# Performance work log

Measured on AMD Instinct MI355X. Metric: run time of the kernel, lower is better.

Reference implementation:

```python
import jax, jax.numpy as jnp
import numpy as np

B, S, E, H, ML = 4, 1024, 1024, 16, 2048
HD = E // H


def setup_inputs() -> dict:
    key = jax.random.key(0)
    ks = jax.random.split(key, 8)
    s = 0.02
    return {
        "x": jax.random.normal(ks[0], (B, S, E), dtype=jnp.float32),
        "rel_pos": jax.random.normal(ks[1], (H, ML), dtype=jnp.float32),
        "in_proj_w": jax.random.normal(ks[2], (3 * E, E), dtype=jnp.float32) * s,
        "in_proj_b": jnp.zeros((3 * E,), jnp.float32),
        "out_w": jax.random.normal(ks[3], (E, E), dtype=jnp.float32) * s,
        "out_b": jnp.zeros((E,), jnp.float32),
        "w1": jax.random.normal(ks[4], (4 * E, E), dtype=jnp.float32) * s,
        "b1": jnp.zeros((4 * E,), jnp.float32),
        "w2": jax.random.normal(ks[5], (E, 4 * E), dtype=jnp.float32) * s,
        "b2": jnp.zeros((E,), jnp.float32),
        "ln1_g": jnp.ones((E,), jnp.float32),
        "ln1_b": jnp.zeros((E,), jnp.float32),
        "ln2_g": jnp.ones((E,), jnp.float32),
        "ln2_b": jnp.zeros((E,), jnp.float32),
    }


def _layernorm(x, g, b, eps=1e-5):
    m = x.mean(-1, keepdims=True)
    v = ((x - m) ** 2).mean(-1, keepdims=True)
    return (x - m) * jax.lax.rsqrt(v + eps) * g + b


def _causal_mask(size, rel_pos):
    # rel_pos: [H, max_len]; size <= max_len branch of the torch code
    flipped = jnp.flip(rel_pos[:, :size], -1)                        # [H, size]
    neg_inf = jnp.full((rel_pos.shape[0], size), -jnp.inf, rel_pos.dtype)
    padded = jnp.concatenate([flipped, neg_inf], axis=-1)            # [H, 2*size]
    idx = jnp.arange(size)[None, :] - jnp.arange(size)[:, None] + size - 1
    return padded[:, idx]                                            # [H, S, S]: rel_pos[i-j] if j<=i else -inf


def reference(x, rel_pos, in_proj_w, in_proj_b, out_w, out_b,
              w1, b1, w2, b2, ln1_g, ln1_b, ln2_g, ln2_b):
    b, s, e = x.shape
    xn = _layernorm(x, ln1_g, ln1_b)
    qkv = xn @ in_proj_w.T + in_proj_b                               # [B,S,3E]
    q, k, v = jnp.split(qkv, 3, axis=-1)
    q = q.reshape(b, s, H, HD).transpose(0, 2, 1, 3)                 # [B,H,S,D]
    k = k.reshape(b, s, H, HD).transpose(0, 2, 1, 3)
    v = v.reshape(b, s, H, HD).transpose(0, 2, 1, 3)
    mask = _causal_mask(s, rel_pos)                                  # [H,S,S], broadcast over batch (== repeat(B,1,1))
    scores = jnp.einsum("bhqd,bhkd->bhqk", q, k) / np.sqrt(HD) + mask[None]
    attn = jax.nn.softmax(scores, axis=-1)
    o = jnp.einsum("bhqk,bhkd->bhqd", attn, v)                       # [B,H,S,D]
    o = o.transpose(0, 2, 1, 3).reshape(b, s, e)
    att_out = o @ out_w.T + out_b
    x = x + att_out
    xm = _layernorm(x, ln2_g, ln2_b)
    mlp = jax.nn.relu(xm @ w1.T + b1) @ w2.T + b2
    return x + mlp
```

## Files before the change

### kernel.cpp

```cpp
#include <hip/hip_runtime.h>
#include <stdint.h>

typedef __bf16 bf16x8 __attribute__((ext_vector_type(8)));
typedef float  f32x4  __attribute__((ext_vector_type(4)));

__device__ __forceinline__ unsigned short f2bf(float f) {
  union { float f; unsigned int u; } a; a.f = f;
  unsigned int r = a.u + 0x7FFFu + ((a.u >> 16) & 1u);
  return (unsigned short)(r >> 16);
}

__device__ __forceinline__ unsigned short f2bf_fast(float f) {
  union { __bf16 b; unsigned short u; } v; v.b = (__bf16)f; return v.u;
}

__device__ __forceinline__ void cp16(const void* g, void* l) {
  auto g1 = reinterpret_cast<__attribute__((address_space(1))) unsigned int*>(
      reinterpret_cast<uintptr_t>(g));
  auto l3 = reinterpret_cast<__attribute__((address_space(3))) unsigned int*>(
      reinterpret_cast<uintptr_t>(l));
  __builtin_amdgcn_global_load_lds(g1, l3, 16, 0, 0);
}

__global__ __launch_bounds__(256) void cvt_bf16(const float* __restrict__ in,
                                                unsigned short* __restrict__ out,
                                                int n) {
  int i = (blockIdx.x * 256 + threadIdx.x) * 4;
  if (i >= n) return;
  float4 v = *(const float4*)(in + i);
  union { unsigned short u[4]; uint2 p; } o;
  o.u[0] = f2bf(v.x); o.u[1] = f2bf(v.y); o.u[2] = f2bf(v.z); o.u[3] = f2bf(v.w);
  *(uint2*)(out + i) = o.p;
}

__global__ __launch_bounds__(256) void init_br(const float* __restrict__ resid,
                                               const float* __restrict__ bias,
                                               float* __restrict__ out) {
  int i = (blockIdx.x * 256 + threadIdx.x) * 4;
  float4 r = *(const float4*)(resid + i);
  float4 b = *(const float4*)(bias + (i & 1023));
  r.x += b.x; r.y += b.y; r.z += b.z; r.w += b.w;
  *(float4*)(out + i) = r;
}

__global__ __launch_bounds__(256) void ln_bf16(const float* __restrict__ x,
                                               const float* __restrict__ g,
                                               const float* __restrict__ bta,
                                               unsigned short* __restrict__ out) {
  const int row = blockIdx.x, t = threadIdx.x;
  const float4 v = *(const float4*)(x + (size_t)row * 1024 + t * 4);
  float s1 = v.x + v.y + v.z + v.w;
  float s2 = v.x*v.x + v.y*v.y + v.z*v.z + v.w*v.w;
  #pragma unroll
  for (int off = 1; off < 64; off <<= 1) {
    s1 += __shfl_xor(s1, off, 64);
    s2 += __shfl_xor(s2, off, 64);
  }
  __shared__ float r1[4], r2[4];
  if ((t & 63) == 0) { r1[t >> 6] = s1; r2[t >> 6] = s2; }
  __syncthreads();
  s1 = r1[0] + r1[1] + r1[2] + r1[3];
  s2 = r2[0] + r2[1] + r2[2] + r2[3];
  const float mean = s1 * (1.0f / 1024.0f);
  const float var  = s2 * (1.0f / 1024.0f) - mean * mean;
  const float rstd = rsqrtf(var + 1e-5f);
  const float4 gv = *(const float4*)(g + t * 4);
  const float4 bv = *(const float4*)(bta + t * 4);
  union { unsigned short u[4]; uint2 p; } o;
  o.u[0] = f2bf((v.x - mean) * rstd * gv.x + bv.x);
  o.u[1] = f2bf((v.y - mean) * rstd * gv.y + bv.y);
  o.u[2] = f2bf((v.z - mean) * rstd * gv.z + bv.z);
  o.u[3] = f2bf((v.w - mean) * rstd * gv.w + bv.w);
  *(uint2*)(out + (size_t)row * 1024 + t * 4) = o.p;
}

template <int MODE>
__global__ __launch_bounds__(256, 2) void gemm_bt(
    const unsigned short* __restrict__ A,
    const unsigned short* __restrict__ Bt,
    const float* __restrict__ bias,
    void* __restrict__ outp,
    int N, int K) {
  __shared__ __align__(16) unsigned short As[128 * 64];
  __shared__ __align__(16) unsigned short Bs[128 * 64];
  const int tid = threadIdx.x;
  const int wave = tid >> 6, lane = tid & 63;
  const int q = lane >> 4, c = lane & 15;
  const int wm = (wave & 1) << 6, wn = (wave >> 1) << 6;
  const int m0 = blockIdx.x << 7, n0 = blockIdx.y << 7;

  const int srow = tid >> 3;
  const int cg8  = ((tid & 7) ^ (srow & 7)) << 3;

  const unsigned short* gA = A  + (size_t)(m0 + srow) * K + cg8;
  const unsigned short* gB = Bt + (size_t)(n0 + srow) * K + cg8;
  unsigned short* lA = &As[tid * 8];
  unsigned short* lB = &Bs[tid * 8];
  const size_t rstep = (size_t)32 * K;

  const f32x4 fzero = {0.f, 0.f, 0.f, 0.f};
  f32x4 acc[4][4];
  #pragma unroll
  for (int i = 0; i < 4; i++)
    #pragma unroll
    for (int j = 0; j < 4; j++) acc[i][j] = fzero;

  for (int k0 = 0; k0 < K; k0 += 64) {
    __syncthreads();
    #pragma unroll
    for (int it = 0; it < 4; it++) {
      cp16(gA + it * rstep + k0, lA + it * 2048);
      cp16(gB + it * rstep + k0, lB + it * 2048);
    }
    __syncthreads();
    #pragma unroll
    for (int ks = 0; ks < 2; ks++) {
      const int sw = (((ks << 2) + q) ^ (c & 7)) << 3;
      bf16x8 af[4], bf[4];
      #pragma unroll
      for (int i = 0; i < 4; i++) af[i] = *(const bf16x8*)&As[(wm + i*16 + c)*64 + sw];
      #pragma unroll
      for (int j = 0; j < 4; j++) bf[j] = *(const bf16x8*)&Bs[(wn + j*16 + c)*64 + sw];
      #pragma unroll
      for (int i = 0; i < 4; i++)
        #pragma unroll
        for (int j = 0; j < 4; j++)
          acc[i][j] = __builtin_amdgcn_mfma_f32_16x16x32_bf16(af[i], bf[j], acc[i][j], 0, 0, 0);
    }
  }

  float bj[4];
  #pragma unroll
  for (int j = 0; j < 4; j++) bj[j] = bias[n0 + wn + j * 16 + c];
  #pragma unroll
  for (int i = 0; i < 4; i++) {
    #pragma unroll
    for (int r = 0; r < 4; r++) {
      const int row = m0 + wm + i * 16 + q * 4 + r;
      #pragma unroll
      for (int j = 0; j < 4; j++) {
        const int col = n0 + wn + j * 16 + c;
        const size_t idx = (size_t)row * N + col;
        float v = acc[i][j][r] + bj[j];
        if (MODE == 0)      ((unsigned short*)outp)[idx] = f2bf(v);
        else                ((unsigned short*)outp)[idx] = f2bf(fmaxf(v, 0.f));
      }
    }
  }
}

__global__ __launch_bounds__(256, 2) void gemm_bt_splitk(
    const unsigned short* __restrict__ A,
    const unsigned short* __restrict__ Bt,
    float* __restrict__ outp,
    int N, int K) {
  __shared__ __align__(16) unsigned short As[128 * 64];
  __shared__ __align__(16) unsigned short Bs[128 * 64];
  const int tid = threadIdx.x;
  const int wave = tid >> 6, lane = tid & 63;
  const int q = lane >> 4, c = lane & 15;
  const int wm = (wave & 1) << 6, wn = (wave >> 1) << 6;
  const int m0 = blockIdx.x << 7, n0 = blockIdx.y << 7;
  const int KH = K >> 1;
  const int kbeg = blockIdx.z * KH, kend = kbeg + KH;

  const int srow = tid >> 3;
  const int cg8  = ((tid & 7) ^ (srow & 7)) << 3;

  const unsigned short* gA = A  + (size_t)(m0 + srow) * K + cg8;
  const unsigned short* gB = Bt + (size_t)(n0 + srow) * K + cg8;
  unsigned short* lA = &As[tid * 8];
  unsigned short* lB = &Bs[tid * 8];
  const size_t rstep = (size_t)32 * K;

  const f32x4 fzero = {0.f, 0.f, 0.f, 0.f};
  f32x4 acc[4][4];
  #pragma unroll
  for (int i = 0; i < 4; i++)
    #pragma unroll
    for (int j = 0; j < 4; j++) acc[i][j] = fzero;

  for (int k0 = kbeg; k0 < kend; k0 += 64) {
    __syncthreads();
    #pragma unroll
    for (int it = 0; it < 4; it++) {
      cp16(gA + it * rstep + k0, lA + it * 2048);
      cp16(gB + it * rstep + k0, lB + it * 2048);
    }
    __syncthreads();
    #pragma unroll
    for (int ks = 0; ks < 2; ks++) {
      const int sw = (((ks << 2) + q) ^ (c & 7)) << 3;
      bf16x8 af[4], bf[4];
      #pragma unroll
      for (int i = 0; i < 4; i++) af[i] = *(const bf16x8*)&As[(wm + i*16 + c)*64 + sw];
      #pragma unroll
      for (int j = 0; j < 4; j++) bf[j] = *(const bf16x8*)&Bs[(wn + j*16 + c)*64 + sw];
      #pragma unroll
      for (int i = 0; i < 4; i++)
        #pragma unroll
        for (int j = 0; j < 4; j++)
          acc[i][j] = __builtin_amdgcn_mfma_f32_16x16x32_bf16(af[i], bf[j], acc[i][j], 0, 0, 0);
    }
  }

  #pragma unroll
  for (int i = 0; i < 4; i++) {
    #pragma unroll
    for (int r = 0; r < 4; r++) {
      const int row = m0 + wm + i * 16 + q * 4 + r;
      #pragma unroll
      for (int j = 0; j < 4; j++) {
        const int col = n0 + wn + j * 16 + c;
        atomicAdd(outp + (size_t)row * N + col, acc[i][j][r]);
      }
    }
  }
}

__global__ __launch_bounds__(256, 2) void attn_flash(
    const unsigned short* __restrict__ qkv,
    const float* __restrict__ rel_pos,
    unsigned short* __restrict__ o) {
  __shared__ __align__(16) unsigned short Qs[128 * 64];
  __shared__ __align__(16) unsigned short Ks[64 * 64];
  __shared__ __align__(16) unsigned short Vs[64 * 64];
  __shared__ __align__(16) unsigned short Ps[4][32 * 64];
  __shared__ float rps[1024];

  const int tid = threadIdx.x;
  const int wave = tid >> 6, lane = tid & 63;
  const int q = lane >> 4, c = lane & 15;

  const int lid = blockIdx.x + (blockIdx.y << 3);
  const int xq = lid & 7, y = lid >> 3;
  const int qt = (y & 32) ? (7 - xq) : xq;
  const int b = y >> 4, h = y & 15;

  const unsigned short* qg = qkv + (size_t)b * 1024 * 3072 + h * 64;
  const unsigned short* kg = qg + 1024;
  const unsigned short* vg = qg + 2048;

  #pragma unroll
  for (int i = 0; i < 4; i++) {
    const int idx = tid + i * 256;
    rps[idx & 1023] = rel_pos[h * 2048 + (idx & 1023)] * 1.44269504f;
  }

  const int sr  = tid >> 3;
  const int cg8 = ((tid & 7) ^ (sr & 7)) << 3;
  #pragma unroll
  for (int it = 0; it < 4; it++)
    cp16(qg + (size_t)(qt * 128 + sr + it * 32) * 3072 + cg8, &Qs[(tid + it * 256) * 8]);
  __syncthreads();

  bf16x8 qf[2][2];
  #pragma unroll
  for (int mt = 0; mt < 2; mt++)
    #pragma unroll
    for (int ks = 0; ks < 2; ks++)
      qf[mt][ks] = *(const bf16x8*)&Qs[(wave*32 + mt*16 + c)*64 + ((((ks<<2)+q) ^ (c & 7)) << 3)];

  const f32x4 fzero = {0.f, 0.f, 0.f, 0.f};
  f32x4 O[2][4];
  float l_i[2][4];
  #pragma unroll
  for (int mt = 0; mt < 2; mt++) {
    #pragma unroll
    for (int r = 0; r < 4; r++) l_i[mt][r] = 0.f;
    #pragma unroll
    for (int dt = 0; dt < 4; dt++) O[mt][dt] = fzero;
  }

  unsigned short* Pw = &Ps[wave][0];
  const int i_base = qt * 128 + wave * 32;
  const int vrow = tid & 63, d0 = (tid >> 6) << 4;
  const int vchunk = vrow >> 3, vlo = vrow & 7;

  const float sc = 0.125f * 1.44269504f;
  const int kdiag = qt << 1;
  const int nkt = (qt + 1) * 2;

  for (int kt = 0; kt < nkt; kt++) {
    __syncthreads();
    cp16(kg + (size_t)(kt * 64 + sr) * 3072 + cg8, &Ks[tid * 8]);
    cp16(kg + (size_t)(kt * 64 + sr + 32) * 3072 + cg8, &Ks[(tid + 256) * 8]);
    {
      union { int4 v; unsigned short u[8]; } va, vb2;
      const unsigned short* vrp = vg + (size_t)(kt * 64 + vrow) * 3072 + d0;
      va.v  = *(const int4*)vrp;
      vb2.v = *(const int4*)(vrp + 8);
      #pragma unroll
      for (int j = 0; j < 8; j++) {
        const int pos = ((vchunk ^ j) << 3) + vlo;
        Vs[(d0 + j) * 64 + pos]     = va.u[j];
        Vs[(d0 + 8 + j) * 64 + pos] = vb2.u[j];
      }
    }
    __syncthreads();

    f32x4 S[2][4];
    #pragma unroll
    for (int mt = 0; mt < 2; mt++)
      #pragma unroll
      for (int nt = 0; nt < 4; nt++) S[mt][nt] = fzero;
    #pragma unroll
    for (int ks = 0; ks < 2; ks++) {
      const int sw = (((ks << 2) + q) ^ (c & 7)) << 3;
      bf16x8 kb[4];
      #pragma unroll
      for (int nt = 0; nt < 4; nt++) kb[nt] = *(const bf16x8*)&Ks[(nt*16 + c)*64 + sw];
      #pragma unroll
      for (int mt = 0; mt < 2; mt++)
        #pragma unroll
        for (int nt = 0; nt < 4; nt++)
          S[mt][nt] = __builtin_amdgcn_mfma_f32_16x16x32_bf16(qf[mt][ks], kb[nt], S[mt][nt], 0, 0, 0);
    }

    if (kt < kdiag) {
      #pragma unroll
      for (int mt = 0; mt < 2; mt++) {
        #pragma unroll
        for (int r = 0; r < 4; r++) {
          const int i_ = i_base + mt * 16 + q * 4 + r;
          const int prow = (mt * 16 + q * 4 + r) * 64;
          const int rsw  = (q * 4 + r) & 7;
          float s = 0.f;
          #pragma unroll
          for (int nt = 0; nt < 4; nt++) {
            const int j_ = kt * 64 + nt * 16 + c;
            const float p = exp2f(fmaf(S[mt][nt][r], sc, rps[i_ - j_]));
            s += p;
            Pw[prow + ((((nt << 1) + (c >> 3)) ^ rsw) << 3) + (c & 7)] = f2bf_fast(p);
          }
          l_i[mt][r] += s;
        }
      }
    } else {
      #pragma unroll
      for (int mt = 0; mt < 2; mt++) {
        #pragma unroll
        for (int r = 0; r < 4; r++) {
          const int i_ = i_base + mt * 16 + q * 4 + r;
          const int prow = (mt * 16 + q * 4 + r) * 64;
          const int rsw  = (q * 4 + r) & 7;
          float s = 0.f;
          #pragma unroll
          for (int nt = 0; nt < 4; nt++) {
            const int j_ = kt * 64 + nt * 16 + c;
            const int d_ = i_ - j_;
            const float p = (d_ >= 0)
                ? exp2f(fmaf(S[mt][nt][r], sc, rps[d_ & 1023])) : 0.f;
            s += p;
            Pw[prow + ((((nt << 1) + (c >> 3)) ^ rsw) << 3) + (c & 7)] = f2bf_fast(p);
          }
          l_i[mt][r] += s;
        }
      }
    }

    asm volatile("s_waitcnt lgkmcnt(0)" ::: "memory");

    #pragma unroll
    for (int ks = 0; ks < 2; ks++) {
      const int sw = (((ks << 2) + q) ^ (c & 7)) << 3;
      bf16x8 pa[2], vb[4];
      #pragma unroll
      for (int mt = 0; mt < 2; mt++) pa[mt] = *(const bf16x8*)&Pw[(mt*16 + c)*64 + sw];
      #pragma unroll
      for (int dt = 0; dt < 4; dt++) vb[dt] = *(const bf16x8*)&Vs[(dt*16 + c)*64 + sw];
      #pragma unroll
      for (int mt = 0; mt < 2; mt++)
        #pragma unroll
        for (int dt = 0; dt < 4; dt++)
          O[mt][dt] = __builtin_amdgcn_mfma_f32_16x16x32_bf16(pa[mt], vb[dt], O[mt][dt], 0, 0, 0);
    }
  }

  #pragma unroll
  for (int mt = 0; mt < 2; mt++) {
    #pragma unroll
    for (int r = 0; r < 4; r++) {
      float l = l_i[mt][r];
      l += __shfl_xor(l, 1, 64);
      l += __shfl_xor(l, 2, 64);
      l += __shfl_xor(l, 4, 64);
      l += __shfl_xor(l, 8, 64);
      const float inv = 1.0f / l;
      const int i_ = i_base + mt * 16 + q * 4 + r;
      unsigned short* orow = o + (size_t)(b * 1024 + i_) * 1024 + h * 64 + c;
      #pragma unroll
      for (int dt = 0; dt < 4; dt++) orow[dt * 16] = f2bf(O[mt][dt][r] * inv);
    }
  }
}

extern "C" void kernel_launch(void* const* d_in, const int* in_sizes, int n_in,
                              void* d_out, int out_size, void* d_ws, size_t ws_size,
                              hipStream_t stream) {
  (void)in_sizes; (void)n_in; (void)out_size; (void)ws_size;
  const float* x    = (const float*)d_in[0];
  const float* rel  = (const float*)d_in[1];
  const float* ipw  = (const float*)d_in[2];
  const float* ipb  = (const float*)d_in[3];
  const float* outw = (const float*)d_in[4];
  const float* outb = (const float*)d_in[5];
  const float* w1   = (const float*)d_in[6];
  const float* b1   = (const float*)d_in[7];
  const float* w2   = (const float*)d_in[8];
  const float* b2   = (const float*)d_in[9];
  const float* ln1g = (const float*)d_in[10];
  const float* ln1b = (const float*)d_in[11];
  const float* ln2g = (const float*)d_in[12];
  const float* ln2b = (const float*)d_in[13];

  unsigned short* ipw_b  = (unsigned short*)d_ws;
  unsigned short* outw_b = ipw_b  + (size_t)3072 * 1024;
  unsigned short* w1_b   = outw_b + (size_t)1024 * 1024;
  unsigned short* w2_b   = w1_b   + (size_t)4096 * 1024;
  unsigned short* xn     = w2_b   + (size_t)1024 * 4096;
  unsigned short* qkvb   = xn     + (size_t)4096 * 1024;
  unsigned short* ob     = qkvb   + (size_t)4096 * 3072;
  float*          x2     = (float*)(ob + (size_t)4096 * 1024);
  unsigned short* xm     = (unsigned short*)(x2 + (size_t)4096 * 1024);
  unsigned short* hb     = xm + (size_t)4096 * 1024;

  cvt_bf16<<<3072 * 1024 / 1024, 256, 0, stream>>>(ipw, ipw_b, 3072 * 1024);
  cvt_bf16<<<1024 * 1024 / 1024, 256, 0, stream>>>(outw, outw_b, 1024 * 1024);
  cvt_bf16<<<4096 * 1024 / 1024, 256, 0, stream>>>(w1, w1_b, 4096 * 1024);
  cvt_bf16<<<4096 * 1024 / 1024, 256, 0, stream>>>(w2, w2_b, 4096 * 1024);

  ln_bf16<<<4096, 256, 0, stream>>>(x, ln1g, ln1b, xn);

  gemm_bt<0><<<dim3(32, 24), 256, 0, stream>>>(xn, ipw_b, ipb, qkvb, 3072, 1024);

  attn_flash<<<dim3(8, 64), 256, 0, stream>>>(qkvb, rel, ob);

  init_br<<<4096, 256, 0, stream>>>(x, outb, x2);
  gemm_bt_splitk<<<dim3(32, 8, 2), 256, 0, stream>>>(ob, outw_b, x2, 1024, 1024);

  ln_bf16<<<4096, 256, 0, stream>>>(x2, ln2g, ln2b, xm);

  gemm_bt<2><<<dim3(32, 32), 256, 0, stream>>>(xm, w1_b, b1, hb, 4096, 1024);

  init_br<<<4096, 256, 0, stream>>>(x2, b2, (float*)d_out);
  gemm_bt_splitk<<<dim3(32, 8, 2), 256, 0, stream>>>(hb, w2_b, (float*)d_out, 1024, 4096);
}
```

Baseline: 347.9 us.

## Merge weight conversions, fold residual seeding into layernorm, deepen split-K

Replaces the four weight-conversion launches with one kernel that selects source and destination by index range. Folds the residual-plus-bias seeding into the layernorm kernels, which removes two init_br launches and one re-read of the activations each. Raises split-K from 2 to 4 ways for both output GEMMs and asks for higher occupancy in launch bounds. This launches more atomic-accumulating blocks, so atomic contention rises and floating-point summation order changes.

```diff
diff --git a/kernel.cpp b/kernel.cpp
--- a/kernel.cpp
+++ b/kernel.cpp
@@ -22,33 +22,39 @@
   __builtin_amdgcn_global_load_lds(g1, l3, 16, 0, 0);
 }
 
-__global__ __launch_bounds__(256) void cvt_bf16(const float* __restrict__ in,
-                                                unsigned short* __restrict__ out,
-                                                int n) {
+__global__ __launch_bounds__(256) void cvt_all(
+    const float* __restrict__ s0, const float* __restrict__ s1,
+    const float* __restrict__ s2, const float* __restrict__ s3,
+    unsigned short* __restrict__ d0, unsigned short* __restrict__ d1,
+    unsigned short* __restrict__ d2, unsigned short* __restrict__ d3) {
   int i = (blockIdx.x * 256 + threadIdx.x) * 4;
-  if (i >= n) return;
-  float4 v = *(const float4*)(in + i);
+  const float* src; unsigned short* dst; int off;
+  if (i < 3145728)       { src = s0; dst = d0; off = 0; }
+  else if (i < 4194304)  { src = s1; dst = d1; off = 3145728; }
+  else if (i < 8388608)  { src = s2; dst = d2; off = 4194304; }
+  else                   { src = s3; dst = d3; off = 8388608; }
+  i -= off;
+  float4 v = *(const float4*)(src + i);
   union { unsigned short u[4]; uint2 p; } o;
   o.u[0] = f2bf(v.x); o.u[1] = f2bf(v.y); o.u[2] = f2bf(v.z); o.u[3] = f2bf(v.w);
-  *(uint2*)(out + i) = o.p;
-}
-
-__global__ __launch_bounds__(256) void init_br(const float* __restrict__ resid,
-                                               const float* __restrict__ bias,
-                                               float* __restrict__ out) {
-  int i = (blockIdx.x * 256 + threadIdx.x) * 4;
-  float4 r = *(const float4*)(resid + i);
-  float4 b = *(const float4*)(bias + (i & 1023));
-  r.x += b.x; r.y += b.y; r.z += b.z; r.w += b.w;
-  *(float4*)(out + i) = r;
-}
-
-__global__ __launch_bounds__(256) void ln_bf16(const float* __restrict__ x,
-                                               const float* __restrict__ g,
-                                               const float* __restrict__ bta,
-                                               unsigned short* __restrict__ out) {
+  *(uint2*)(dst + i) = o.p;
+}
+
+__global__ __launch_bounds__(256) void ln_bf16_seed(
+    const float* __restrict__ x,
+    const float* __restrict__ g,
+    const float* __restrict__ bta,
+    unsigned short* __restrict__ out,
+    const float* __restrict__ seed_bias,
+    float* __restrict__ seed_out) {
   const int row = blockIdx.x, t = threadIdx.x;
   const float4 v = *(const float4*)(x + (size_t)row * 1024 + t * 4);
+  {
+    float4 sb = *(const float4*)(seed_bias + t * 4);
+    float4 sv;
+    sv.x = v.x + sb.x; sv.y = v.y + sb.y; sv.z = v.z + sb.z; sv.w = v.w + sb.w;
+    *(float4*)(seed_out + (size_t)row * 1024 + t * 4) = sv;
+  }
   float s1 = v.x + v.y + v.z + v.w;
   float s2 = v.x*v.x + v.y*v.y + v.z*v.z + v.w*v.w;
   #pragma unroll
@@ -149,11 +155,11 @@
   }
 }
 
-__global__ __launch_bounds__(256, 2) void gemm_bt_splitk(
+__global__ __launch_bounds__(256, 4) void gemm_bt_splitk(
     const unsigned short* __restrict__ A,
     const unsigned short* __restrict__ Bt,
     float* __restrict__ outp,
-    int N, int K) {
+    int N, int K, int KH) {
   __shared__ __align__(16) unsigned short As[128 * 64];
   __shared__ __align__(16) unsigned short Bs[128 * 64];
   const int tid = threadIdx.x;
@@ -161,7 +167,6 @@
   const int q = lane >> 4, c = lane & 15;
   const int wm = (wave & 1) << 6, wn = (wave >> 1) << 6;
   const int m0 = blockIdx.x << 7, n0 = blockIdx.y << 7;
-  const int KH = K >> 1;
   const int kbeg = blockIdx.z * KH, kend = kbeg + KH;
 
   const int srow = tid >> 3;
@@ -425,24 +430,19 @@
   unsigned short* xm     = (unsigned short*)(x2 + (size_t)4096 * 1024);
   unsigned short* hb     = xm + (size_t)4096 * 1024;
 
-  cvt_bf16<<<3072 * 1024 / 1024, 256, 0, stream>>>(ipw, ipw_b, 3072 * 1024);
-  cvt_bf16<<<1024 * 1024 / 1024, 256, 0, stream>>>(outw, outw_b, 1024 * 1024);
-  cvt_bf16<<<4096 * 1024 / 1024, 256, 0, stream>>>(w1, w1_b, 4096 * 1024);
-  cvt_bf16<<<4096 * 1024 / 1024, 256, 0, stream>>>(w2, w2_b, 4096 * 1024);
-
-  ln_bf16<<<4096, 256, 0, stream>>>(x, ln1g, ln1b, xn);
+  cvt_all<<<12288, 256, 0, stream>>>(ipw, outw, w1, w2, ipw_b, outw_b, w1_b, w2_b);
+
+  ln_bf16_seed<<<4096, 256, 0, stream>>>(x, ln1g, ln1b, xn, outb, x2);
 
   gemm_bt<0><<<dim3(32, 24), 256, 0, stream>>>(xn, ipw_b, ipb, qkvb, 3072, 1024);
 
   attn_flash<<<dim3(8, 64), 256, 0, stream>>>(qkvb, rel, ob);
 
-  init_br<<<4096, 256, 0, stream>>>(x, outb, x2);
-  gemm_bt_splitk<<<dim3(32, 8, 2), 256, 0, stream>>>(ob, outw_b, x2, 1024, 1024);
-
-  ln_bf16<<<4096, 256, 0, stream>>>(x2, ln2g, ln2b, xm);
+  gemm_bt_splitk<<<dim3(32, 8, 4), 256, 0, stream>>>(ob, outw_b, x2, 1024, 1024, 256);
+
+  ln_bf16_seed<<<4096, 256, 0, stream>>>(x2, ln2g, ln2b, xm, b2, (float*)d_out);
 
   gemm_bt<2><<<dim3(32, 32), 256, 0, stream>>>(xm, w1_b, b1, hb, 4096, 1024);
 
-  init_br<<<4096, 256, 0, stream>>>(x2, b2, (float*)d_out);
-  gemm_bt_splitk<<<dim3(32, 8, 2), 256, 0, stream>>>(hb, w2_b, (float*)d_out, 1024, 4096);
-}
+  gemm_bt_splitk<<<dim3(32, 8, 4), 256, 0, stream>>>(hb, w2_b, (float*)d_out, 1024, 4096, 1024);
+}
```

New measurement: 371.1 us. 6.7% more time.
